# Performance work log

Measured on AMD Instinct MI355X. Metric: run time of the kernel, lower is better.

## Reference

```python
import jax, jax.numpy as jnp
import numpy as np

THETA0 = 3.0
THETA = 5.0
R = 5  # window radius == theta; the sdf is clipped to [-theta, theta], so distances beyond R are saturated

# all integer offsets within Euclidean radius THETA (78 of them)
_OFFSETS = [(dy, dx, float(np.hypot(dy, dx)))
            for dy in range(-R, R + 1) for dx in range(-R, R + 1)
            if np.hypot(dy, dx) <= THETA]


def _capped_edt(target_set):
    """target_set: bool [B,H,W]. Min Euclidean distance from each pixel to a True
    pixel, capped at THETA (exact for all values that survive the later clip)."""
    B, H, W = target_set.shape
    pad = jnp.pad(target_set, ((0, 0), (R, R), (R, R)), constant_values=False)
    d = jnp.full((B, H, W), THETA, dtype=jnp.float32)
    for dy, dx, dist in _OFFSETS:
        win = pad[:, R + dy:R + dy + H, R + dx:R + dx + W]
        d = jnp.minimum(d, jnp.where(win, jnp.float32(dist), jnp.float32(THETA)))
    return d


def _compute_sdf(mask):
    """mask: float [B,H,W]. Mirrors BoundaryLoss.compute_sdf:
    sdf_pos = edt(1-mask) = dist to nearest pixel where mask==1 (zeros of 1-mask)
    sdf_neg = edt(mask)   = dist to nearest pixel where mask==0
    (the `boundary` tensor in the torch code is computed but never used)."""
    sdf_pos = _capped_edt(mask == 1.0)
    sdf_neg = _capped_edt(mask == 0.0)
    sdf = jnp.clip(sdf_pos - sdf_neg, -THETA, THETA) / THETA
    empty = jnp.sum(mask, axis=(1, 2)) == 0.0  # per-batch empty-mask branch -> theta0
    return jnp.where(empty[:, None, None], jnp.float32(THETA0), sdf)


def _boundary_loss(pred, target):
    p = jax.nn.softmax(pred, axis=1)  # [B,C,H,W]
    C = pred.shape[1]
    loss = jnp.float32(0.0)
    for c in range(C):  # small fixed class count
        pred_sdf = _compute_sdf(p[:, c])
        tgt_sdf = _compute_sdf((target == c).astype(jnp.float32))
        loss = loss + jnp.mean(jnp.abs(pred_sdf - tgt_sdf))  # F.l1_loss, mean
    return loss / C


def setup_inputs() -> dict:
    key = jax.random.key(0)
    k1, k2 = jax.random.split(key)
    pred = jax.random.normal(k1, (16, 4, 512, 512), dtype=jnp.float32)
    target = jax.random.randint(k2, (16, 512, 512), 0, 4, dtype=jnp.int32)
    return {"pred": pred, "target": target}


def reference(pred, target):
    return _boundary_loss(pred, target)
```

## Files before the change

### kernel.cpp

```cpp
#include <hip/hip_runtime.h>
#include <stdint.h>

#define BB 16
#define CC 4
#define HH 512
#define WW 512
#define NWORDS 8
#define HW (HH * WW)

#define OFF_FLAGS 64
#define OFF_MODE  1024
#define OFF_TGT   4096
#define BOARD_BYTES (CC * BB * HH * NWORDS * 8)

__global__ void build_bits(const int* __restrict__ tgt,
                           const float* __restrict__ pred,
                           uint64_t* __restrict__ tgtb,
                           uint64_t* __restrict__ ppos,
                           uint64_t* __restrict__ pneg,
                           double* __restrict__ acc) {
    int row = blockIdx.x;
    int b = row >> 9, y = row & (HH - 1);
    int x = threadIdx.x;
    if (row == 0 && x == 0) *acc = 0.0;

    int t = tgt[((size_t)(b * HH + y)) * WW + x];
    size_t i0 = (((size_t)b * CC) * HH + y) * (size_t)WW + x;
    float a0 = pred[i0];
    float a1 = pred[i0 + (size_t)HW];
    float a2 = pred[i0 + 2 * (size_t)HW];
    float a3 = pred[i0 + 3 * (size_t)HW];
    float m = fmaxf(fmaxf(a0, a1), fmaxf(a2, a3));
    float e0 = expf(a0 - m), e1 = expf(a1 - m), e2 = expf(a2 - m), e3 = expf(a3 - m);
    float s = (e0 + e1) + (e2 + e3);
    float p0 = e0 / s, p1 = e1 / s, p2 = e2 / s, p3 = e3 / s;

    int wv = x >> 6;
    bool l0 = (x & 63) == 0;
#define EMIT(cidx, pv)                                                        \
    {                                                                         \
        uint64_t mt = __ballot(t == (cidx));                                  \
        uint64_t mp = __ballot((pv) == 1.0f);                                 \
        uint64_t mn = __ballot((pv) == 0.0f);                                 \
        if (l0) {                                                             \
            size_t o = (((size_t)(cidx) * BB + b) * HH + y) * NWORDS + wv;    \
            tgtb[o] = mt;                                                     \
            ppos[o] = mp;                                                     \
            pneg[o] = mn;                                                     \
        }                                                                     \
    }
    EMIT(0, p0)
    EMIT(1, p1)
    EMIT(2, p2)
    EMIT(3, p3)
#undef EMIT
}

__global__ void flags_kernel(const uint64_t* __restrict__ tgtb,
                             const uint64_t* __restrict__ pposb,
                             const uint64_t* __restrict__ pnegb,
                             unsigned* __restrict__ flags,
                             unsigned* __restrict__ mode,
                             double* __restrict__ acc) {
    int cb = blockIdx.x;
    const uint64_t* t  = tgtb  + (size_t)cb * HH * NWORDS;
    const uint64_t* pp = pposb + (size_t)cb * HH * NWORDS;
    const uint64_t* pn = pnegb + (size_t)cb * HH * NWORDS;
    uint64_t ot = 0ull, op = 0ull, on = 0ull, an = ~0ull;
    for (int i = threadIdx.x; i < HH * NWORDS; i += blockDim.x) {
        ot |= t[i];
        op |= pp[i];
        uint64_t v = pn[i];
        on |= v;
        an &= v;
    }
    for (int s = 32; s > 0; s >>= 1) {
        ot |= (uint64_t)__shfl_down((unsigned long long)ot, s, 64);
        op |= (uint64_t)__shfl_down((unsigned long long)op, s, 64);
        on |= (uint64_t)__shfl_down((unsigned long long)on, s, 64);
        an &= (uint64_t)__shfl_down((unsigned long long)an, s, 64);
    }
    __shared__ uint64_t sot[8], sop[8], son[8], san[8];
    int wv = threadIdx.x >> 6;
    if ((threadIdx.x & 63) == 0) { sot[wv]=ot; sop[wv]=op; son[wv]=on; san[wv]=an; }
    __syncthreads();
    if (threadIdx.x == 0) {
        int nw = blockDim.x >> 6;
        uint64_t OT = 0, OP = 0, ON = 0, AN = ~0ull;
        for (int i = 0; i < nw; ++i) { OT|=sot[i]; OP|=sop[i]; ON|=son[i]; AN&=san[i]; }
        unsigned present = (OT != 0ull)  ? 1u : 0u;
        unsigned prednz  = (AN != ~0ull) ? 1u : 0u;
        unsigned fast    = (OP == 0ull && ON == 0ull) ? 1u : 0u;
        flags[cb]      = present;
        flags[64 + cb] = prednz;
        mode[cb]       = fast;
        if (fast && !present) atomicAdd(acc, 3.0 * (double)HW);
    }
}

__device__ __forceinline__ constexpr int lev_idx(int d2) {
    return d2==0?0: d2==1?1: d2==2?2: d2==4?3: d2==5?4: d2==8?5: d2==9?6:
           d2==10?7: d2==13?8: d2==16?9: d2==17?10: d2==18?11: d2==20?12: 13;
}

__device__ __forceinline__ unsigned win11(const uint64_t* row10, int idx, int p) {
    uint64_t w;
    if (p < 64) {
        w = (row10[idx] >> p) | (row10[idx + 1] << (64 - p));
    } else {
        int q = p - 64;
        uint64_t M = row10[idx + 1];
        w = q ? ((M >> q) | (row10[idx + 2] << (64 - q))) : M;
    }
    return (unsigned)w & 0x7FFu;
}

__device__ __forceinline__ void upd(int& mind2, unsigned wbits, int dy2) {
    if (wbits) {
        unsigned hi = wbits >> 5;
        unsigned lo = wbits & 31u;
        int mdx = 6;
        if (hi) mdx = __ffs(hi) - 1;
        if (lo) {
            int m2 = 5 - (31 - __clz(lo));
            mdx = min(mdx, m2);
        }
        int cand = dy2 + mdx * mdx;
        mind2 = min(mind2, cand);
    }
}

__launch_bounds__(512)
__global__ void edt_main(const uint64_t* __restrict__ tgtb,
                         const uint64_t* __restrict__ pposb,
                         const uint64_t* __restrict__ pnegb,
                         const unsigned* __restrict__ flags,
                         const unsigned* __restrict__ mode,
                         double* __restrict__ acc) {
    __shared__ uint64_t shm[74 * 8];
    __shared__ float wsum[8];
    int tile = blockIdx.x & 7;
    int cb   = blockIdx.x >> 3;
    int y0   = tile * 64;

    if (mode[cb]) {
        if (!flags[cb]) return;
        uint64_t (*sT)[8] = (uint64_t (*)[8])shm;
        const uint64_t* board = tgtb + (size_t)cb * HH * NWORDS;
        for (int t = threadIdx.x; t < 74 * 8; t += 512) {
            int r = t >> 3, w = t & 7;
            int yy = y0 + r - 5;
            sT[r][w] = (yy >= 0 && yy < HH) ? board[(size_t)yy * NWORDS + w] : 0ull;
        }
        __syncthreads();

        int tr = threadIdx.x >> 3;
        int w  = threadIdx.x & 7;
        int y  = y0 + tr;

        uint64_t DT[14], DC[14];
#pragma unroll
        for (int k = 0; k < 14; ++k) { DT[k] = 0ull; DC[k] = 0ull; }

#pragma unroll
        for (int dy = -5; dy <= 5; ++dy) {
            int yy = y + dy;
            if (yy < 0 || yy >= HH) continue;
            const int ady  = dy < 0 ? -dy : dy;
            const int maxs = (ady == 0) ? 5 : (ady <= 3) ? 4 : (ady == 4) ? 3 : 0;
            int ly = tr + 5 + dy;
            uint64_t Cw = sT[ly][w];
            uint64_t Lw = (w > 0) ? sT[ly][w - 1] : 0ull;
            uint64_t Rw = (w < 7) ? sT[ly][w + 1] : 0ull;
            uint64_t Cc = ~Cw;
            uint64_t Lc = (w > 0) ? ~Lw : 0ull;
            uint64_t Rc = (w < 7) ? ~Rw : 0ull;
            uint64_t UT = Cw, UC = Cc;
            DT[lev_idx(ady * ady)] |= UT;
            DC[lev_idx(ady * ady)] |= UC;
#pragma unroll
            for (int s = 1; s <= 5; ++s) {
                if (s > maxs) break;
                UT |= (Cw >> s) | (Rw << (64 - s)) | (Cw << s) | (Lw >> (64 - s));
                UC |= (Cc >> s) | (Rc << (64 - s)) | (Cc << s) | (Lc >> (64 - s));
                const int li = lev_idx(ady * ady + s * s);
                DT[li] |= UT;
                DC[li] |= UC;
            }
        }

        const float dist[14] = {0.f, 1.f, 1.41421356f, 2.f, 2.23606798f,
            2.82842712f, 3.f, 3.16227766f, 3.60555128f, 4.f, 4.12310563f,
            4.24264069f, 4.47213595f, 5.f};
        uint64_t covT = 0ull, covC = 0ull;
        float s = 0.f;
#pragma unroll
        for (int k = 0; k < 14; ++k) {
            uint64_t nT = DT[k] & ~covT;
            uint64_t nC = DC[k] & ~covC;
            s += dist[k] * (float)(__popcll(nT) + __popcll(nC));
            covT |= DT[k];
            covC |= DC[k];
        }
        s += 5.f * (float)(__popcll(~covT) + __popcll(~covC));

        for (int o = 32; o > 0; o >>= 1) s += __shfl_down(s, o, 64);
        if ((threadIdx.x & 63) == 0) wsum[threadIdx.x >> 6] = s;
        __syncthreads();
        if (threadIdx.x == 0) {
            float tot = 0.f;
#pragma unroll
            for (int i = 0; i < 8; ++i) tot += wsum[i];
            atomicAdd(acc, (double)tot * 0.2);
        }
        return;
    }

    uint64_t (*sh)[11][10] = (uint64_t (*)[11][10])shm;
    int x = threadIdx.x;
    int idx = x >> 6, off = x & 63, p = off + 59;
    int b = cb & (BB - 1);
    int c = cb >> 4;
    unsigned fpres = flags[cb], fnz = flags[64 + cb];

    unsigned vmask = 0x7FFu;
    if (x < 5) vmask &= (0x7FFu << (5 - x)) & 0x7FFu;
    if (x > WW - 6) vmask &= 0x7FFu >> (x - (WW - 6));

    float vsum = 0.f;
    for (int yy = 0; yy < 64; ++yy) {
        int y = y0 + yy;
        __syncthreads();
        for (int t = threadIdx.x; t < 330; t += 512) {
            int m = t / 110;
            int rem = t - m * 110;
            int r = rem / 10;
            int wi = rem - r * 10;
            int rowy = y + r - 5;
            uint64_t v = 0;
            if (wi >= 1 && wi <= 8 && rowy >= 0 && rowy < HH) {
                const uint64_t* src = (m == 0) ? tgtb : (m == 1) ? pposb : pnegb;
                v = src[(((size_t)c * BB + b) * HH + rowy) * NWORDS + (wi - 1)];
            }
            sh[m][r][wi] = v;
        }
        __syncthreads();

        int tp = 26, tn = 26, qp = 26, qn = 26;
#pragma unroll
        for (int dy = -5; dy <= 5; ++dy) {
            int ady = dy < 0 ? -dy : dy;
            unsigned allowed = (ady == 0) ? 0x7FFu
                             : (ady <= 3) ? 0x3FEu
                             : (ady == 4) ? 0x1FCu
                                          : 0x020u;
            int dy2 = dy * dy;
            int r = dy + 5;
            unsigned wt  = win11(&sh[0][r][0], idx, p);
            unsigned wpp = win11(&sh[1][r][0], idx, p);
            unsigned wpn = win11(&sh[2][r][0], idx, p);
            upd(tp, wt & allowed, dy2);
            upd(tn, (~wt) & vmask & allowed, dy2);
            upd(qp, wpp & allowed, dy2);
            upd(qn, wpn & allowed, dy2);
        }

        float dtp = (tp <= 25) ? sqrtf((float)tp) : 5.0f;
        float dtn = (tn <= 25) ? sqrtf((float)tn) : 5.0f;
        float dqp = (qp <= 25) ? sqrtf((float)qp) : 5.0f;
        float dqn = (qn <= 25) ? sqrtf((float)qn) : 5.0f;

        float td = fminf(fmaxf(dtp - dtn, -5.0f), 5.0f) / 5.0f;
        float qd = fminf(fmaxf(dqp - dqn, -5.0f), 5.0f) / 5.0f;
        float tsdf = fpres ? td : 3.0f;
        float psdf = fnz ? qd : 3.0f;
        vsum += fabsf(psdf - tsdf);
    }

    for (int o2 = 32; o2 > 0; o2 >>= 1) vsum += __shfl_down(vsum, o2, 64);
    if (off == 0) wsum[idx] = vsum;
    __syncthreads();
    if (threadIdx.x == 0) {
        float s = 0.f;
#pragma unroll
        for (int i = 0; i < 8; ++i) s += wsum[i];
        atomicAdd(acc, (double)s);
    }
}

__global__ void finalize_kernel(const double* __restrict__ acc, float* __restrict__ out) {
    out[0] = (float)(acc[0] / 16777216.0);
}

extern "C" void kernel_launch(void* const* d_in, const int* in_sizes, int n_in,
                              void* d_out, int out_size, void* d_ws, size_t ws_size,
                              hipStream_t stream) {
    const float* pred  = (const float*)d_in[0];
    const int* target  = (const int*)d_in[1];
    float* out = (float*)d_out;

    char* ws = (char*)d_ws;
    double*   acc   = (double*)ws;
    unsigned* flags = (unsigned*)(ws + OFF_FLAGS);
    unsigned* mode  = (unsigned*)(ws + OFF_MODE);
    uint64_t* tgtb  = (uint64_t*)(ws + OFF_TGT);
    uint64_t* pposb = (uint64_t*)(ws + OFF_TGT + (size_t)BOARD_BYTES);
    uint64_t* pnegb = (uint64_t*)(ws + OFF_TGT + 2 * (size_t)BOARD_BYTES);

    hipLaunchKernelGGL(build_bits, dim3(BB * HH), dim3(512), 0, stream,
                       target, pred, tgtb, pposb, pnegb, acc);
    hipLaunchKernelGGL(flags_kernel, dim3(CC * BB), dim3(512), 0, stream,
                       tgtb, pposb, pnegb, flags, mode, acc);
    hipLaunchKernelGGL(edt_main, dim3(CC * BB * 8), dim3(512), 0, stream,
                       tgtb, pposb, pnegb, flags, mode, acc);
    hipLaunchKernelGGL(finalize_kernel, dim3(1), dim3(1), 0, stream, acc, out);
}
```

Before: 132.9 us.

## Fold flag reduction into build_bits and edt_main, drop two kernels

Each build_bits block now writes a per-row summary word (target present, any pred==1, any pred==0, all pred==0). Each edt_main block reduces the 512 row summaries for its class/batch itself, replacing the separate flags_kernel. Accumulation now goes straight into the float output with pre-scaled atomics, which removes the finalize kernel and the double accumulator. This cuts two kernel launches and a full re-read of the bitboards, at the cost of redundant flag reductions per tile and float instead of double atomic accumulation, which may lose some precision.

```diff
diff --git a/kernel.cpp b/kernel.cpp
--- a/kernel.cpp
+++ b/kernel.cpp
@@ -8,9 +8,8 @@
 #define NWORDS 8
 #define HW (HH * WW)
 
-#define OFF_FLAGS 64
-#define OFF_MODE  1024
-#define OFF_TGT   4096
+#define OFF_ROW   1024
+#define OFF_TGT   262144
 #define BOARD_BYTES (CC * BB * HH * NWORDS * 8)
 
 __global__ void build_bits(const int* __restrict__ tgt,
@@ -18,11 +17,13 @@
                            uint64_t* __restrict__ tgtb,
                            uint64_t* __restrict__ ppos,
                            uint64_t* __restrict__ pneg,
-                           double* __restrict__ acc) {
+                           unsigned* __restrict__ rowsum,
+                           float* __restrict__ out) {
+    __shared__ unsigned srow[CC][8];
     int row = blockIdx.x;
     int b = row >> 9, y = row & (HH - 1);
     int x = threadIdx.x;
-    if (row == 0 && x == 0) *acc = 0.0;
+    if (row == 0 && x == 0) out[0] = 0.0f;
 
     int t = tgt[((size_t)(b * HH + y)) * WW + x];
     size_t i0 = (((size_t)b * CC) * HH + y) * (size_t)WW + x;
@@ -47,6 +48,8 @@
             tgtb[o] = mt;                                                     \
             ppos[o] = mp;                                                     \
             pneg[o] = mn;                                                     \
+            srow[cidx][wv] = (mt != 0ull ? 1u : 0u) | (mp != 0ull ? 2u : 0u)  \
+                           | (mn != 0ull ? 4u : 0u) | (mn == ~0ull ? 8u : 0u);\
         }                                                                     \
     }
     EMIT(0, p0)
@@ -54,47 +57,12 @@
     EMIT(2, p2)
     EMIT(3, p3)
 #undef EMIT
-}
-
-__global__ void flags_kernel(const uint64_t* __restrict__ tgtb,
-                             const uint64_t* __restrict__ pposb,
-                             const uint64_t* __restrict__ pnegb,
-                             unsigned* __restrict__ flags,
-                             unsigned* __restrict__ mode,
-                             double* __restrict__ acc) {
-    int cb = blockIdx.x;
-    const uint64_t* t  = tgtb  + (size_t)cb * HH * NWORDS;
-    const uint64_t* pp = pposb + (size_t)cb * HH * NWORDS;
-    const uint64_t* pn = pnegb + (size_t)cb * HH * NWORDS;
-    uint64_t ot = 0ull, op = 0ull, on = 0ull, an = ~0ull;
-    for (int i = threadIdx.x; i < HH * NWORDS; i += blockDim.x) {
-        ot |= t[i];
-        op |= pp[i];
-        uint64_t v = pn[i];
-        on |= v;
-        an &= v;
-    }
-    for (int s = 32; s > 0; s >>= 1) {
-        ot |= (uint64_t)__shfl_down((unsigned long long)ot, s, 64);
-        op |= (uint64_t)__shfl_down((unsigned long long)op, s, 64);
-        on |= (uint64_t)__shfl_down((unsigned long long)on, s, 64);
-        an &= (uint64_t)__shfl_down((unsigned long long)an, s, 64);
-    }
-    __shared__ uint64_t sot[8], sop[8], son[8], san[8];
-    int wv = threadIdx.x >> 6;
-    if ((threadIdx.x & 63) == 0) { sot[wv]=ot; sop[wv]=op; son[wv]=on; san[wv]=an; }
     __syncthreads();
-    if (threadIdx.x == 0) {
-        int nw = blockDim.x >> 6;
-        uint64_t OT = 0, OP = 0, ON = 0, AN = ~0ull;
-        for (int i = 0; i < nw; ++i) { OT|=sot[i]; OP|=sop[i]; ON|=son[i]; AN&=san[i]; }
-        unsigned present = (OT != 0ull)  ? 1u : 0u;
-        unsigned prednz  = (AN != ~0ull) ? 1u : 0u;
-        unsigned fast    = (OP == 0ull && ON == 0ull) ? 1u : 0u;
-        flags[cb]      = present;
-        flags[64 + cb] = prednz;
-        mode[cb]       = fast;
-        if (fast && !present) atomicAdd(acc, 3.0 * (double)HW);
+    if (x < CC) {
+        unsigned o = 0u, a = 8u;
+#pragma unroll
+        for (int i = 0; i < 8; ++i) { o |= srow[x][i]; a &= srow[x][i]; }
+        rowsum[((size_t)x * BB + b) * HH + y] = (o & 7u) | a;
     }
 }
 
@@ -134,17 +102,48 @@
 __global__ void edt_main(const uint64_t* __restrict__ tgtb,
                          const uint64_t* __restrict__ pposb,
                          const uint64_t* __restrict__ pnegb,
-                         const unsigned* __restrict__ flags,
-                         const unsigned* __restrict__ mode,
-                         double* __restrict__ acc) {
+                         const unsigned* __restrict__ rowsum,
+                         float* __restrict__ out) {
     __shared__ uint64_t shm[74 * 8];
     __shared__ float wsum[8];
+    __shared__ unsigned sflag[8];
     int tile = blockIdx.x & 7;
     int cb   = blockIdx.x >> 3;
     int y0   = tile * 64;
-
-    if (mode[cb]) {
-        if (!flags[cb]) return;
+    const float INV_N = 1.0f / 16777216.0f;
+
+    {
+        unsigned rs = rowsum[(size_t)cb * HH + threadIdx.x];
+        uint64_t bT = __ballot((rs & 1u) != 0u);
+        uint64_t bP = __ballot((rs & 2u) != 0u);
+        uint64_t bN = __ballot((rs & 4u) != 0u);
+        uint64_t bAllNot = __ballot((rs & 8u) == 0u);
+        if ((threadIdx.x & 63) == 0)
+            sflag[threadIdx.x >> 6] = (bT ? 1u : 0u) | (bP ? 2u : 0u)
+                                    | (bN ? 4u : 0u) | (bAllNot ? 8u : 0u);
+        __syncthreads();
+        if (threadIdx.x == 0) {
+            unsigned o = 0u;
+#pragma unroll
+            for (int i = 0; i < 8; ++i) o |= sflag[i];
+            sflag[0] = o;
+        }
+        __syncthreads();
+    }
+    unsigned F = sflag[0];
+    bool present  = (F & 1u) != 0u;
+    bool anyppos  = (F & 2u) != 0u;
+    bool anypneg  = (F & 4u) != 0u;
+    bool prednz   = (F & 8u) != 0u;
+    bool fast     = !anyppos && !anypneg;
+    __syncthreads();
+
+    if (fast) {
+        if (!present) {
+            if (tile == 0 && threadIdx.x == 0)
+                atomicAdd(out, 3.0f * (float)HW * INV_N);
+            return;
+        }
         uint64_t (*sT)[8] = (uint64_t (*)[8])shm;
         const uint64_t* board = tgtb + (size_t)cb * HH * NWORDS;
         for (int t = threadIdx.x; t < 74 * 8; t += 512) {
@@ -211,7 +210,7 @@
             float tot = 0.f;
 #pragma unroll
             for (int i = 0; i < 8; ++i) tot += wsum[i];
-            atomicAdd(acc, (double)tot * 0.2);
+            atomicAdd(out, tot * 0.2f * INV_N);
         }
         return;
     }
@@ -221,7 +220,6 @@
     int idx = x >> 6, off = x & 63, p = off + 59;
     int b = cb & (BB - 1);
     int c = cb >> 4;
-    unsigned fpres = flags[cb], fnz = flags[64 + cb];
 
     unsigned vmask = 0x7FFu;
     if (x < 5) vmask &= (0x7FFu << (5 - x)) & 0x7FFu;
@@ -272,8 +270,8 @@
 
         float td = fminf(fmaxf(dtp - dtn, -5.0f), 5.0f) / 5.0f;
         float qd = fminf(fmaxf(dqp - dqn, -5.0f), 5.0f) / 5.0f;
-        float tsdf = fpres ? td : 3.0f;
-        float psdf = fnz ? qd : 3.0f;
+        float tsdf = present ? td : 3.0f;
+        float psdf = prednz ? qd : 3.0f;
         vsum += fabsf(psdf - tsdf);
     }
 
@@ -284,12 +282,8 @@
         float s = 0.f;
 #pragma unroll
         for (int i = 0; i < 8; ++i) s += wsum[i];
-        atomicAdd(acc, (double)s);
-    }
-}
-
-__global__ void finalize_kernel(const double* __restrict__ acc, float* __restrict__ out) {
-    out[0] = (float)(acc[0] / 16777216.0);
+        atomicAdd(out, s * INV_N);
+    }
 }
 
 extern "C" void kernel_launch(void* const* d_in, const int* in_sizes, int n_in,
@@ -300,18 +294,13 @@
     float* out = (float*)d_out;
 
     char* ws = (char*)d_ws;
-    double*   acc   = (double*)ws;
-    unsigned* flags = (unsigned*)(ws + OFF_FLAGS);
-    unsigned* mode  = (unsigned*)(ws + OFF_MODE);
-    uint64_t* tgtb  = (uint64_t*)(ws + OFF_TGT);
-    uint64_t* pposb = (uint64_t*)(ws + OFF_TGT + (size_t)BOARD_BYTES);
-    uint64_t* pnegb = (uint64_t*)(ws + OFF_TGT + 2 * (size_t)BOARD_BYTES);
+    unsigned* rowsum = (unsigned*)(ws + OFF_ROW);
+    uint64_t* tgtb   = (uint64_t*)(ws + OFF_TGT);
+    uint64_t* pposb  = (uint64_t*)(ws + OFF_TGT + (size_t)BOARD_BYTES);
+    uint64_t* pnegb  = (uint64_t*)(ws + OFF_TGT + 2 * (size_t)BOARD_BYTES);
 
     hipLaunchKernelGGL(build_bits, dim3(BB * HH), dim3(512), 0, stream,
-                       target, pred, tgtb, pposb, pnegb, acc);
-    hipLaunchKernelGGL(flags_kernel, dim3(CC * BB), dim3(512), 0, stream,
-                       tgtb, pposb, pnegb, flags, mode, acc);
+                       target, pred, tgtb, pposb, pnegb, rowsum, out);
     hipLaunchKernelGGL(edt_main, dim3(CC * BB * 8), dim3(512), 0, stream,
-                       tgtb, pposb, pnegb, flags, mode, acc);
-    hipLaunchKernelGGL(finalize_kernel, dim3(1), dim3(1), 0, stream, acc, out);
-}
+                       tgtb, pposb, pnegb, rowsum, out);
+}
```

Result: faster. 126.8 us, median of 2 (-4.6%).
